# Optimization experiments

Hardware: AMD Instinct MI355X
Metric: run time of the kernel (lower is better)

## Reference

```python
import math
import jax, jax.numpy as jnp
import numpy as np

N_HEAD = 32
HEAD_DIM = 64
ROTARY_DIM = 32
ROTARY_BASE = 10000.0


def _rope(u, cos, sin):
    # u: [B, S, H, head_dim]; cos/sin: [S, ROTARY_DIM//2]
    u_rot = u[..., :ROTARY_DIM].astype(jnp.float32)
    u1, u2 = jnp.split(u_rot, 2, axis=-1)          # [B,S,H,rot/2] each
    c = cos[None, :, None, :]
    s = sin[None, :, None, :]
    r = jnp.concatenate([u1 * c - u2 * s, u1 * s + u2 * c], axis=-1).astype(u.dtype)
    return jnp.concatenate([r, u[..., ROTARY_DIM:]], axis=-1)


def setup_inputs() -> dict:
    key = jax.random.key(0)
    ks = jax.random.split(key, 5)
    B, S, D = 2, 2048, 2048
    std = 1.0 / math.sqrt(D)
    x = jax.random.normal(ks[0], (B, S, D), dtype=jnp.float32)
    Wqkv = jax.random.normal(ks[1], (D, 3 * D), dtype=jnp.float32) * std
    b_qkv = jax.random.normal(ks[2], (3 * D,), dtype=jnp.float32) * 0.01
    Wout = jax.random.normal(ks[3], (D, D), dtype=jnp.float32) * std
    b_out = jax.random.normal(ks[4], (D,), dtype=jnp.float32) * 0.01
    return {"x": x, "Wqkv": Wqkv, "b_qkv": b_qkv, "Wout": Wout, "b_out": b_out}


def reference(x, Wqkv, b_qkv, Wout, b_out):
    B, S, D = x.shape
    H, hd = N_HEAD, HEAD_DIM
    # QKV projection -> [B, S, 3, H, hd]
    qkv = (x @ Wqkv + b_qkv).reshape(B, S, 3, H, hd)
    # Rotary cos/sin cache (fp32 position indices, as in the module)
    inv_freq = 1.0 / (ROTARY_BASE ** (jnp.arange(0, ROTARY_DIM, 2, dtype=jnp.float32) / ROTARY_DIM))
    t = jnp.arange(S, dtype=jnp.float32)
    freqs = jnp.outer(t, inv_freq)                 # [S, ROTARY_DIM//2]
    cos, sin = jnp.cos(freqs), jnp.sin(freqs)
    q = _rope(qkv[:, :, 0], cos, sin)
    k = _rope(qkv[:, :, 1], cos, sin)
    v = qkv[:, :, 2]
    scale = 1.0 / math.sqrt(hd)
    scores = jnp.einsum('bthd,bshd->bhts', q, k * scale)   # [B,H,S,S]
    rows = jnp.arange(S)[:, None]
    cols = jnp.arange(S)[None, :]
    causal_mask = cols > rows                      # seqlen_k == seqlen_q here
    scores = jnp.where(causal_mask[None, None], jnp.asarray(-10000.0, scores.dtype), scores)
    attn = jax.nn.softmax(scores, axis=-1)         # dropout p=0.0
    out = jnp.einsum('bhts,bshd->bthd', attn, v).reshape(B, S, D)
    return out @ Wout + b_out
```

## Files before the change

kernel.cpp:

```cpp
#include <hip/hip_runtime.h>
#include <stdint.h>
#include <math.h>

#define DEV static __device__ __forceinline__

typedef __attribute__((ext_vector_type(8))) short bf16x8;
typedef __attribute__((ext_vector_type(4))) float f32x4;
typedef __attribute__((ext_vector_type(8))) unsigned short u16x8;
typedef __attribute__((ext_vector_type(4))) unsigned short u16x4;
typedef __attribute__((ext_vector_type(2))) unsigned int u32x2;

enum { B_ = 2, S_ = 2048, D_ = 2048, H_ = 32, HD_ = 64, N3_ = 6144, M_ = 4096 };

DEV unsigned short f2bf(float f) {
  unsigned u = __float_as_uint(f);
  u += 0x7FFFu + ((u >> 16) & 1u);
  return (unsigned short)(u >> 16);
}
DEV float bf2f(unsigned short s) { return __uint_as_float(((unsigned)s) << 16); }

DEV void load16(const void* g, void* l) {
  __builtin_amdgcn_global_load_lds((const __attribute__((address_space(1))) void*)g,
                                   (__attribute__((address_space(3))) void*)l,
                                   16, 0, 0);
}

DEV f32x4 mfma16(bf16x8 a, bf16x8 b, f32x4 c) {
  return __builtin_amdgcn_mfma_f32_16x16x32_bf16(a, b, c, 0, 0, 0);
}

__global__ __launch_bounds__(256) void cvt_bf16(const float* __restrict__ in,
                                                unsigned short* __restrict__ out, int n) {
  int i = blockIdx.x * 256 + threadIdx.x;
  if (i * 8 >= n) return;
  const float4* in4 = (const float4*)in;
  float4 a = in4[i * 2 + 0];
  float4 b = in4[i * 2 + 1];
  u16x8 o;
  o[0] = f2bf(a.x); o[1] = f2bf(a.y); o[2] = f2bf(a.z); o[3] = f2bf(a.w);
  o[4] = f2bf(b.x); o[5] = f2bf(b.y); o[6] = f2bf(b.z); o[7] = f2bf(b.w);
  *(u16x8*)(out + (size_t)i * 8) = o;
}

__global__ __launch_bounds__(256) void transpose_bf16(const float* __restrict__ W,
                                                      unsigned short* __restrict__ Wt,
                                                      int Kg, int Ng) {
  __shared__ float tile[32][33];
  const int tn = blockIdx.x, tk = blockIdx.y;
  const int t = threadIdx.x;
  const int r = t >> 3, c4 = (t & 7) * 4;
  float4 v = *(const float4*)(W + (size_t)(tk * 32 + r) * Ng + tn * 32 + c4);
  tile[r][c4 + 0] = v.x; tile[r][c4 + 1] = v.y;
  tile[r][c4 + 2] = v.z; tile[r][c4 + 3] = v.w;
  __syncthreads();
  u16x4 o;
  o[0] = f2bf(tile[c4 + 0][r]);
  o[1] = f2bf(tile[c4 + 1][r]);
  o[2] = f2bf(tile[c4 + 2][r]);
  o[3] = f2bf(tile[c4 + 3][r]);
  *(u16x4*)(Wt + (size_t)(tn * 32 + r) * Kg + tk * 32 + c4) = o;
}

DEV int xsw(int row) { return (row ^ (row >> 2)) & 3; }

template <int MODE>
__global__ __launch_bounds__(256) void gemm_bt(const unsigned short* __restrict__ A,
                                               const unsigned short* __restrict__ BT,
                                               const float* __restrict__ bias,
                                               void* __restrict__ Cout,
                                               unsigned short* __restrict__ vt,
                                               int Mg, int Ng, int Kg) {
  __shared__ __align__(16) unsigned short lA[128 * 32];
  __shared__ __align__(16) unsigned short lB[128 * 32];
  const int tid = threadIdx.x;
  const int lane = tid & 63, wv = tid >> 6;
  const int g = lane >> 4, l16 = lane & 15;
  const int wr = wv >> 1, wc = wv & 1;
  const int rb = blockIdx.x * 128, cb = blockIdx.y * 128;

  f32x4 acc[4][4] = {};

  for (int k0 = 0; k0 < Kg; k0 += 32) {
    __syncthreads();
#pragma unroll
    for (int c = 0; c < 2; ++c) {
      int p = c * 256 + tid;
      int row = p >> 2;
      int k8l = (p & 3) ^ xsw(row);
      load16(A + (size_t)(rb + row) * Kg + k0 + 8 * k8l, (char*)lA + p * 16);
      load16(BT + (size_t)(cb + row) * Kg + k0 + 8 * k8l, (char*)lB + p * 16);
    }
    __syncthreads();
    bf16x8 af[4], bfr[4];
#pragma unroll
    for (int m = 0; m < 4; ++m) {
      int row = wr * 64 + m * 16 + l16;
      af[m] = *(const bf16x8*)((const char*)lA + (size_t)(row * 4 + (g ^ xsw(row))) * 16);
    }
#pragma unroll
    for (int n = 0; n < 4; ++n) {
      int row = wc * 64 + n * 16 + l16;
      bfr[n] = *(const bf16x8*)((const char*)lB + (size_t)(row * 4 + (g ^ xsw(row))) * 16);
    }
#pragma unroll
    for (int m = 0; m < 4; ++m)
#pragma unroll
      for (int n = 0; n < 4; ++n)
        acc[m][n] = mfma16(af[m], bfr[n], acc[m][n]);
  }

  const int ccol0 = cb + wc * 64 + l16;
  float bv[4];
#pragma unroll
  for (int n = 0; n < 4; ++n) bv[n] = bias[ccol0 + n * 16];

  if (MODE == 1) {
    const int cblk = cb + wc * 64;
    if (cblk >= 4096) {
      const int hv = (cblk - 4096) >> 6;
#pragma unroll
      for (int m = 0; m < 4; ++m) {
        int row = rb + wr * 64 + m * 16 + g * 4;
        int b = row >> 11, s0 = row & (S_ - 1);
#pragma unroll
        for (int n = 0; n < 4; ++n) {
          u16x4 ov;
#pragma unroll
          for (int r = 0; r < 4; ++r) ov[r] = f2bf(acc[m][n][r] + bv[n]);
          *(u16x4*)(vt + ((size_t)(b * 32 + hv) * 64 + n * 16 + l16) * S_ + s0) = ov;
        }
      }
    } else {
      unsigned short* O = (unsigned short*)Cout;
      const float invf = exp2f(-(float)l16 * 0.83048202372184056f);
#pragma unroll
      for (int m = 0; m < 4; ++m)
#pragma unroll
        for (int r = 0; r < 4; ++r) {
          int row = rb + wr * 64 + m * 16 + g * 4 + r;
          float v0 = acc[m][0][r] + bv[0];
          float v1 = acc[m][1][r] + bv[1];
          float v2 = acc[m][2][r] + bv[2];
          float v3 = acc[m][3][r] + bv[3];
          float ang = (float)(row & (S_ - 1)) * invf;
          float sn = __sinf(ang), cs = __cosf(ang);
          float t0 = v0 * cs - v1 * sn;
          v1 = v0 * sn + v1 * cs;
          v0 = t0;
          unsigned short* p = O + (size_t)row * Ng + ccol0;
          p[0] = f2bf(v0); p[16] = f2bf(v1); p[32] = f2bf(v2); p[48] = f2bf(v3);
        }
    }
  } else {
    float* O = (float*)Cout;
#pragma unroll
    for (int m = 0; m < 4; ++m)
#pragma unroll
      for (int r = 0; r < 4; ++r) {
        int row = rb + wr * 64 + m * 16 + g * 4 + r;
        float* p = O + (size_t)row * Ng + ccol0;
        p[0] = acc[m][0][r] + bv[0];
        p[16] = acc[m][1][r] + bv[1];
        p[32] = acc[m][2][r] + bv[2];
        p[48] = acc[m][3][r] + bv[3];
      }
  }
}

DEV void stage_kv(const unsigned short* __restrict__ qkv,
                  const unsigned short* __restrict__ vt,
                  unsigned char* lds, int bS, int bh64, int hoff, int kvb, int buf, int tid) {
#pragma unroll
  for (int c = 0; c < 2; ++c) {
    int p = c * 256 + tid;
    int row = p >> 3, k8 = (p & 7) ^ (row & 7);
    load16(qkv + (size_t)(bS + kvb + row) * N3_ + 2048 + hoff + 8 * k8,
           lds + buf * 8192 + p * 16);
    load16(vt + (size_t)(bh64 + row) * S_ + kvb + 8 * k8,
           lds + 16384 + buf * 8192 + p * 16);
  }
}

__global__ __launch_bounds__(256, 3) void attn_kernel(const unsigned short* __restrict__ qkv,
                                                      const unsigned short* __restrict__ vt,
                                                      unsigned short* __restrict__ ao) {
  __shared__ __align__(16) unsigned char lds[49152];
  const int tid = threadIdx.x;
  const int lane = tid & 63, wv = tid >> 6;
  const int g = lane >> 4, l16 = lane & 15;
  const int bid = blockIdx.x;
  const int qi = 15 - (bid >> 6);
  const int t6 = bid & 63;
  const int bh = ((t6 & 7) << 3) | (t6 >> 3);
  const int b = bh >> 5, h = bh & 31;
  const int qbase = qi * 128;
  const int srow0 = qbase + wv * 32;
  const int bS = b * S_, bh64 = bh * 64, hoff = h * 64;

  bf16x8 qf[2][2];
#pragma unroll
  for (int m = 0; m < 2; ++m)
#pragma unroll
    for (int kt = 0; kt < 2; ++kt)
      qf[m][kt] = *(const bf16x8*)(qkv + (size_t)(bS + srow0 + m * 16 + l16) * N3_ +
                                   hoff + kt * 32 + g * 8);

  float mrun[2] = {-INFINITY, -INFINITY}, lrun[2] = {0.f, 0.f};
  f32x4 o[2][4] = {};
  unsigned char* pw = lds + 32768 + wv * 4096;

  const int nkv = (qbase + 128) >> 6;
  stage_kv(qkv, vt, lds, bS, bh64, hoff, 0, 0, tid);
  __syncthreads();

  for (int kb = 0; kb < nkv; ++kb) {
    const int cur = kb & 1;
    if (kb + 1 < nkv) stage_kv(qkv, vt, lds, bS, bh64, hoff, (kb + 1) << 6, cur ^ 1, tid);
    const int kvb = kb << 6;
    if (kvb <= srow0 + 31) {
      const unsigned char* kbuf = lds + cur * 8192;
      const unsigned char* vbuf = lds + 16384 + cur * 8192;

      f32x4 sc[2][4];
#pragma unroll
      for (int n = 0; n < 4; ++n) {
        int row = n * 16 + l16;
        bf16x8 kf0 = *(const bf16x8*)(kbuf + (row * 8 + ((g + 0) ^ (row & 7))) * 16);
        bf16x8 kf1 = *(const bf16x8*)(kbuf + (row * 8 + ((g + 4) ^ (row & 7))) * 16);
#pragma unroll
        for (int m = 0; m < 2; ++m) {
          f32x4 z = {};
          z = mfma16(kf0, qf[m][0], z);
          z = mfma16(kf1, qf[m][1], z);
          sc[m][n] = z;
        }
      }

      const bool boundary = (kvb + 63 > srow0);
#pragma unroll
      for (int m = 0; m < 2; ++m) {
        const int qrow = srow0 + m * 16 + l16;
        if (boundary) {
#pragma unroll
          for (int n = 0; n < 4; ++n)
#pragma unroll
            for (int r = 0; r < 4; ++r) {
              int k = kvb + n * 16 + g * 4 + r;
              if (k > qrow) sc[m][n][r] = -INFINITY;
            }
        }
        float mx = fmaxf(fmaxf(sc[m][0][0], sc[m][0][1]), fmaxf(sc[m][0][2], sc[m][0][3]));
#pragma unroll
        for (int n = 1; n < 4; ++n)
          mx = fmaxf(mx, fmaxf(fmaxf(sc[m][n][0], sc[m][n][1]), fmaxf(sc[m][n][2], sc[m][n][3])));
        mx = fmaxf(mx, __shfl_xor(mx, 16));
        mx = fmaxf(mx, __shfl_xor(mx, 32));
        float pm = mx * 0.125f;
        if (!__all(pm <= mrun[m] + 8.0f)) {
          float mn = fmaxf(mrun[m], pm);
          float al = exp2f((mrun[m] - mn) * 1.44269504f);
          mrun[m] = mn; lrun[m] *= al;
#pragma unroll
          for (int d = 0; d < 4; ++d) o[m][d] *= al;
        }
        const float mt = mrun[m] * 1.44269504f;
        float p[4][4]; float rs = 0.f;
#pragma unroll
        for (int n = 0; n < 4; ++n)
#pragma unroll
          for (int r = 0; r < 4; ++r) {
            p[n][r] = exp2f(fmaf(sc[m][n][r], 0.18033688011112042f, -mt));
            rs += p[n][r];
          }
        rs += __shfl_xor(rs, 16);
        rs += __shfl_xor(rs, 32);
        lrun[m] += rs;
#pragma unroll
        for (int n = 0; n < 4; ++n) {
          unsigned lo, hi;
          asm("v_cvt_pk_bf16_f32 %0, %1, %2" : "=v"(lo) : "v"(p[n][0]), "v"(p[n][1]));
          asm("v_cvt_pk_bf16_f32 %0, %1, %2" : "=v"(hi) : "v"(p[n][2]), "v"(p[n][3]));
          int su = (n * 4 + g) ^ ((l16 & 7) << 1);
          u32x2 wq; wq[0] = lo; wq[1] = hi;
          *(u32x2*)(pw + ((m * 16 + l16) * 16 + su) * 8) = wq;
        }
      }

      bf16x8 pf[2][2];
#pragma unroll
      for (int m = 0; m < 2; ++m)
#pragma unroll
        for (int kt = 0; kt < 2; ++kt) {
          int su = (kt * 8 + g * 2) ^ ((l16 & 7) << 1);
          pf[m][kt] = *(const bf16x8*)(pw + ((m * 16 + l16) * 16 + su) * 8);
        }
#pragma unroll
      for (int dblk = 0; dblk < 4; ++dblk) {
        int row = dblk * 16 + l16;
        bf16x8 vf0 = *(const bf16x8*)(vbuf + (row * 8 + ((g + 0) ^ (row & 7))) * 16);
        bf16x8 vf1 = *(const bf16x8*)(vbuf + (row * 8 + ((g + 4) ^ (row & 7))) * 16);
#pragma unroll
        for (int m = 0; m < 2; ++m) {
          o[m][dblk] = mfma16(vf0, pf[m][0], o[m][dblk]);
          o[m][dblk] = mfma16(vf1, pf[m][1], o[m][dblk]);
        }
      }
    }
    __syncthreads();
  }

#pragma unroll
  for (int m = 0; m < 2; ++m) {
    float inv = 1.0f / lrun[m];
    int q = srow0 + m * 16 + l16;
#pragma unroll
    for (int dblk = 0; dblk < 4; ++dblk) {
      u16x4 ov;
#pragma unroll
      for (int r = 0; r < 4; ++r) ov[r] = f2bf(o[m][dblk][r] * inv);
      *(u16x4*)(ao + (size_t)(bS + q) * D_ + hoff + dblk * 16 + g * 4) = ov;
    }
  }
}

extern "C" void kernel_launch(void* const* d_in, const int* in_sizes, int n_in,
                              void* d_out, int out_size, void* d_ws, size_t ws_size,
                              hipStream_t stream) {
  const float* x = (const float*)d_in[0];
  const float* Wqkv = (const float*)d_in[1];
  const float* bqkv = (const float*)d_in[2];
  const float* Wout = (const float*)d_in[3];
  const float* bout = (const float*)d_in[4];
  float* out = (float*)d_out;

  char* ws = (char*)d_ws;
  unsigned short* Xb = (unsigned short*)(ws + 0);
  unsigned short* Wqkvt = (unsigned short*)(ws + 16777216);
  unsigned short* Woutt = (unsigned short*)(ws + 41943040);
  unsigned short* QKVb = (unsigned short*)(ws + 50331648);
  unsigned short* Vt = (unsigned short*)(ws + 100663296);
  unsigned short* AO = Xb;

  cvt_bf16<<<4096, 256, 0, stream>>>(x, Xb, M_ * D_);
  transpose_bf16<<<dim3(192, 64), 256, 0, stream>>>(Wqkv, Wqkvt, 2048, 6144);
  transpose_bf16<<<dim3(64, 64), 256, 0, stream>>>(Wout, Woutt, 2048, 2048);
  gemm_bt<1><<<dim3(32, 48), 256, 0, stream>>>(Xb, Wqkvt, bqkv, QKVb, Vt, M_, N3_, D_);
  attn_kernel<<<1024, 256, 0, stream>>>(QKVb, Vt, AO);
  gemm_bt<0><<<dim3(32, 16), 256, 0, stream>>>(AO, Woutt, bout, out, nullptr, M_, D_, D_);
}
```

Measured before the change: 290.1 us.

## Add dedicated 256x192 double-buffered QKV GEMM with fine-grained load/MFMA interleaving

Replaces the generic 128x128 QKV projection GEMM with a dedicated 512-thread kernel. Each block computes a 256x192 tile with a K-step of 64, double-buffered LDS fed by direct global-to-LDS loads, split barriers, explicit vmcnt/lgkmcnt waits and raised wave priority during MFMA bursts. Blocks are remapped with an XCD-aware swizzle. Column assignment per wave is arranged so RoPE pairs land in the same wave, and the epilogue keeps the RoPE, bias and V-transpose fusion. The aim is more operand reuse and better overlap of memory and matrix work in the largest GEMM, at the cost of large LDS use, heavy register pressure and hand-tuned wait counts that must match the issued loads exactly.

Measured after the change: 265.1 us. 1.09x faster.

```diff
diff --git a/kernel.cpp b/kernel.cpp
--- a/kernel.cpp
+++ b/kernel.cpp
@@ -61,15 +61,176 @@
   *(u16x4*)(Wt + (size_t)(tn * 32 + r) * Kg + tk * 32 + c4) = o;
 }
 
+__global__ __launch_bounds__(512, 2) void gemm_qkv(const unsigned short* __restrict__ A,
+                                                   const unsigned short* __restrict__ BT,
+                                                   const float* __restrict__ bias,
+                                                   unsigned short* __restrict__ Oqk,
+                                                   unsigned short* __restrict__ vt,
+                                                   int Mg, int Ng, int Kg) {
+  __shared__ __align__(16) char lds[114688];
+  const int tid = threadIdx.x;
+  const int lane = tid & 63, w = tid >> 6;
+  const int g = (lane >> 4) & 3, l16 = lane & 15;
+  const int wm = w >> 2, wn = w & 3;
+
+  const int wg = (blockIdx.x & 7) * (gridDim.x >> 3) + (blockIdx.x >> 3);
+  const int nTM = Mg >> 8;
+  const int tm = wg % nTM, tn = wg / nTM;
+  const int rb = tm * 256, cb = tn * 192;
+  const int NT = Kg >> 6;
+
+  int c0, c1, c2;
+  if (wn == 0)      { c0 = 0;   c1 = 16;  c2 = 32;  }
+  else if (wn == 1) { c0 = 64;  c1 = 80;  c2 = 48;  }
+  else if (wn == 2) { c0 = 128; c1 = 144; c2 = 96;  }
+  else              { c0 = 112; c1 = 160; c2 = 176; }
+
+  const int su0 = (g ^ (l16 & 7)) * 16;
+  const int su1 = ((4 + g) ^ (l16 & 7)) * 16;
+  const int offA = (wm * 128 + l16) * 128;
+  const int offB0 = 32768 + (c0 + l16) * 128;
+  const int offB1 = 32768 + (c1 + l16) * 128;
+  const int offB2 = 32768 + (c2 + l16) * 128;
+
+  const int r0 = tid >> 3;
+  const int u8e = ((tid & 7) ^ (r0 & 7)) * 8;
+  const unsigned short* sAa = A + (size_t)(rb + r0) * Kg + u8e;
+  const unsigned short* sBb = BT + (size_t)(cb + r0) * Kg + u8e;
+  const size_t rs64 = (size_t)Kg * 64;
+  const int dstb = tid * 16;
+
+  auto SA0 = [&](int t) { char* db = (char*)lds + ((t & 1) ? 57344 : 0);
+    load16(sAa + (size_t)t * 64, db + dstb);
+    load16(sAa + 2 * rs64 + (size_t)t * 64, db + 16384 + dstb); };
+  auto SA1 = [&](int t) { char* db = (char*)lds + ((t & 1) ? 57344 : 0);
+    load16(sAa + 1 * rs64 + (size_t)t * 64, db + 8192 + dstb);
+    load16(sAa + 3 * rs64 + (size_t)t * 64, db + 24576 + dstb); };
+  auto SB = [&](int t) { char* db = (char*)lds + ((t & 1) ? 57344 : 0) + 32768;
+    load16(sBb + (size_t)t * 64, db + dstb);
+    load16(sBb + 1 * rs64 + (size_t)t * 64, db + 8192 + dstb);
+    load16(sBb + 2 * rs64 + (size_t)t * 64, db + 16384 + dstb); };
+
+  SA0(0); SA1(0); SB(0); SA0(1); SB(1);
+  asm volatile("s_waitcnt vmcnt(5)" ::: "memory");
+  __builtin_amdgcn_s_barrier();
+
+  f32x4 acc[8][3] = {};
+  bf16x8 a[4][2], b[3][2];
+
+  for (int t = 0; t < NT; ++t) {
+    const char* bs = (const char*)lds + ((t & 1) ? 57344 : 0);
+#pragma unroll
+    for (int mf = 0; mf < 4; ++mf) {
+      a[mf][0] = *(const bf16x8*)(bs + offA + mf * 2048 + su0);
+      a[mf][1] = *(const bf16x8*)(bs + offA + mf * 2048 + su1);
+    }
+    b[0][0] = *(const bf16x8*)(bs + offB0 + su0);
+    b[0][1] = *(const bf16x8*)(bs + offB0 + su1);
+    b[1][0] = *(const bf16x8*)(bs + offB1 + su0);
+    b[1][1] = *(const bf16x8*)(bs + offB1 + su1);
+    b[2][0] = *(const bf16x8*)(bs + offB2 + su0);
+    b[2][1] = *(const bf16x8*)(bs + offB2 + su1);
+    if (t + 1 < NT) SA1(t + 1);
+    asm volatile("s_waitcnt lgkmcnt(8)" ::: "memory");
+    __builtin_amdgcn_s_barrier();
+    asm volatile("s_waitcnt lgkmcnt(0)" ::: "memory");
+    __builtin_amdgcn_s_setprio(1);
+#pragma unroll
+    for (int mf = 0; mf < 4; ++mf)
+#pragma unroll
+      for (int nf = 0; nf < 3; ++nf)
+#pragma unroll
+        for (int kh = 0; kh < 2; ++kh)
+          acc[mf][nf] = mfma16(a[mf][kh], b[nf][kh], acc[mf][nf]);
+    __builtin_amdgcn_s_setprio(0);
+    __builtin_amdgcn_s_barrier();
+    if (t == NT - 1) asm volatile("s_waitcnt vmcnt(0)" ::: "memory");
+    else             asm volatile("s_waitcnt vmcnt(7)" ::: "memory");
+#pragma unroll
+    for (int mf = 0; mf < 4; ++mf) {
+      a[mf][0] = *(const bf16x8*)(bs + offA + (mf + 4) * 2048 + su0);
+      a[mf][1] = *(const bf16x8*)(bs + offA + (mf + 4) * 2048 + su1);
+    }
+    if (t + 2 < NT) { SA0(t + 2); SB(t + 2); }
+    __builtin_amdgcn_s_barrier();
+    asm volatile("s_waitcnt lgkmcnt(0)" ::: "memory");
+    __builtin_amdgcn_s_setprio(1);
+#pragma unroll
+    for (int mf = 0; mf < 4; ++mf)
+#pragma unroll
+      for (int nf = 0; nf < 3; ++nf)
+#pragma unroll
+        for (int kh = 0; kh < 2; ++kh)
+          acc[mf + 4][nf] = mfma16(a[mf][kh], b[nf][kh], acc[mf + 4][nf]);
+    __builtin_amdgcn_s_setprio(0);
+    if (t + 2 < NT)      asm volatile("s_waitcnt vmcnt(7)" ::: "memory");
+    else if (t + 1 < NT) asm volatile("s_waitcnt vmcnt(2)" ::: "memory");
+    __builtin_amdgcn_s_barrier();
+  }
+
+  const int crow0 = rb + wm * 128 + g * 4;
+  const float bv0 = bias[cb + c0 + l16];
+  const float bv1 = bias[cb + c1 + l16];
+  const float bv2 = bias[cb + c2 + l16];
+  const bool rotp = (wn < 3) && (cb + c0 < 4096);
+  const float invf = exp2f(-(float)l16 * 0.83048202372184056f);
+
+#define STOREG(NF, CG, BV) do {                                                \
+    const int col0_ = cb + (CG);                                               \
+    if (col0_ >= 4096) {                                                       \
+      const int hv_ = (col0_ - 4096) >> 6;                                     \
+      const int dd_ = (col0_ & 63) + l16;                                      \
+      _Pragma("unroll")                                                        \
+      for (int mf = 0; mf < 8; ++mf) {                                         \
+        int rowb_ = crow0 + mf * 16;                                           \
+        int bb_ = rowb_ >> 11, s0_ = rowb_ & (S_ - 1);                         \
+        u16x4 ov_;                                                             \
+        _Pragma("unroll")                                                      \
+        for (int r = 0; r < 4; ++r) ov_[r] = f2bf(acc[mf][NF][r] + (BV));      \
+        *(u16x4*)(vt + ((size_t)(bb_ * 32 + hv_) * 64 + dd_) * S_ + s0_) = ov_;\
+      }                                                                        \
+    } else {                                                                   \
+      _Pragma("unroll")                                                        \
+      for (int mf = 0; mf < 8; ++mf)                                           \
+        _Pragma("unroll")                                                      \
+        for (int r = 0; r < 4; ++r) {                                          \
+          int row_ = crow0 + mf * 16 + r;                                      \
+          Oqk[(size_t)row_ * Ng + col0_ + l16] = f2bf(acc[mf][NF][r] + (BV));  \
+        }                                                                      \
+    }                                                                          \
+  } while (0)
+
+  if (rotp) {
+#pragma unroll
+    for (int mf = 0; mf < 8; ++mf)
+#pragma unroll
+      for (int r = 0; r < 4; ++r) {
+        int row = crow0 + mf * 16 + r;
+        float v0 = acc[mf][0][r] + bv0;
+        float v1 = acc[mf][1][r] + bv1;
+        float ang = (float)(row & (S_ - 1)) * invf;
+        float sn = __sinf(ang), cs = __cosf(ang);
+        float t0 = v0 * cs - v1 * sn;
+        v1 = v0 * sn + v1 * cs;
+        unsigned short* p = Oqk + (size_t)row * Ng;
+        p[cb + c0 + l16] = f2bf(t0);
+        p[cb + c1 + l16] = f2bf(v1);
+      }
+  } else {
+    STOREG(0, c0, bv0);
+    STOREG(1, c1, bv1);
+  }
+  STOREG(2, c2, bv2);
+#undef STOREG
+}
+
 DEV int xsw(int row) { return (row ^ (row >> 2)) & 3; }
 
-template <int MODE>
-__global__ __launch_bounds__(256) void gemm_bt(const unsigned short* __restrict__ A,
-                                               const unsigned short* __restrict__ BT,
-                                               const float* __restrict__ bias,
-                                               void* __restrict__ Cout,
-                                               unsigned short* __restrict__ vt,
-                                               int Mg, int Ng, int Kg) {
+__global__ __launch_bounds__(256) void gemm_bt_f32(const unsigned short* __restrict__ A,
+                                                   const unsigned short* __restrict__ BT,
+                                                   const float* __restrict__ bias,
+                                                   float* __restrict__ Cout,
+                                                   int Mg, int Ng, int Kg) {
   __shared__ __align__(16) unsigned short lA[128 * 32];
   __shared__ __align__(16) unsigned short lB[128 * 32];
   const int tid = threadIdx.x;
@@ -113,58 +274,17 @@
   float bv[4];
 #pragma unroll
   for (int n = 0; n < 4; ++n) bv[n] = bias[ccol0 + n * 16];
-
-  if (MODE == 1) {
-    const int cblk = cb + wc * 64;
-    if (cblk >= 4096) {
-      const int hv = (cblk - 4096) >> 6;
-#pragma unroll
-      for (int m = 0; m < 4; ++m) {
-        int row = rb + wr * 64 + m * 16 + g * 4;
-        int b = row >> 11, s0 = row & (S_ - 1);
-#pragma unroll
-        for (int n = 0; n < 4; ++n) {
-          u16x4 ov;
-#pragma unroll
-          for (int r = 0; r < 4; ++r) ov[r] = f2bf(acc[m][n][r] + bv[n]);
-          *(u16x4*)(vt + ((size_t)(b * 32 + hv) * 64 + n * 16 + l16) * S_ + s0) = ov;
-        }
-      }
-    } else {
-      unsigned short* O = (unsigned short*)Cout;
-      const float invf = exp2f(-(float)l16 * 0.83048202372184056f);
-#pragma unroll
-      for (int m = 0; m < 4; ++m)
-#pragma unroll
-        for (int r = 0; r < 4; ++r) {
-          int row = rb + wr * 64 + m * 16 + g * 4 + r;
-          float v0 = acc[m][0][r] + bv[0];
-          float v1 = acc[m][1][r] + bv[1];
-          float v2 = acc[m][2][r] + bv[2];
-          float v3 = acc[m][3][r] + bv[3];
-          float ang = (float)(row & (S_ - 1)) * invf;
-          float sn = __sinf(ang), cs = __cosf(ang);
-          float t0 = v0 * cs - v1 * sn;
-          v1 = v0 * sn + v1 * cs;
-          v0 = t0;
-          unsigned short* p = O + (size_t)row * Ng + ccol0;
-          p[0] = f2bf(v0); p[16] = f2bf(v1); p[32] = f2bf(v2); p[48] = f2bf(v3);
-        }
-    }
-  } else {
-    float* O = (float*)Cout;
-#pragma unroll
-    for (int m = 0; m < 4; ++m)
-#pragma unroll
-      for (int r = 0; r < 4; ++r) {
-        int row = rb + wr * 64 + m * 16 + g * 4 + r;
-        float* p = O + (size_t)row * Ng + ccol0;
-        p[0] = acc[m][0][r] + bv[0];
-        p[16] = acc[m][1][r] + bv[1];
-        p[32] = acc[m][2][r] + bv[2];
-        p[48] = acc[m][3][r] + bv[3];
-      }
-  }
+#pragma unroll
+  for (int m = 0; m < 4; ++m)
+#pragma unroll
+    for (int r = 0; r < 4; ++r) {
+      int row = rb + wr * 64 + m * 16 + g * 4 + r;
+      float* p = Cout + (size_t)row * Ng + ccol0;
+      p[0] = acc[m][0][r] + bv[0];
+      p[16] = acc[m][1][r] + bv[1];
+      p[32] = acc[m][2][r] + bv[2];
+      p[48] = acc[m][3][r] + bv[3];
+    }
 }
 
 DEV void stage_kv(const unsigned short* __restrict__ qkv,
@@ -344,7 +464,7 @@
   cvt_bf16<<<4096, 256, 0, stream>>>(x, Xb, M_ * D_);
   transpose_bf16<<<dim3(192, 64), 256, 0, stream>>>(Wqkv, Wqkvt, 2048, 6144);
   transpose_bf16<<<dim3(64, 64), 256, 0, stream>>>(Wout, Woutt, 2048, 2048);
-  gemm_bt<1><<<dim3(32, 48), 256, 0, stream>>>(Xb, Wqkvt, bqkv, QKVb, Vt, M_, N3_, D_);
+  gemm_qkv<<<512, 512, 0, stream>>>(Xb, Wqkvt, bqkv, QKVb, Vt, M_, N3_, D_);
   attn_kernel<<<1024, 256, 0, stream>>>(QKVb, Vt, AO);
-  gemm_bt<0><<<dim3(32, 16), 256, 0, stream>>>(AO, Woutt, bout, out, nullptr, M_, D_, D_);
-}
+  gemm_bt_f32<<<dim3(32, 16), 256, 0, stream>>>(AO, Woutt, bout, out, M_, D_, D_);
+}
```
